# Kernel optimization log

Hardware: AMD Instinct MI355X
Metric: run time of the kernel (lower is better)

Reference implementation:

```python
import jax, jax.numpy as jnp
import numpy as np

B, S, D, N, H, K = 32, 512, 2048, 16, 128, 64
EPS = 1e-6


def setup_inputs() -> dict:
    key = jax.random.key(0)
    ks = jax.random.split(key, 8)
    # glorot-uniform-like scale for the (D, N, H) attention kernels
    kern_scale = (6.0 / (D + H)) ** 0.5
    down_sd = 1.0 / K  # matches module: mean 0, sd = 1/downsampling_k
    q = jax.random.normal(ks[0], (B, S, D), dtype=jnp.float32)
    k = jax.random.normal(ks[1], (B, S, D), dtype=jnp.float32)
    v = jax.random.normal(ks[2], (B, S, D), dtype=jnp.float32)
    query_kernel = jax.random.uniform(ks[3], (D, N, H), jnp.float32, -kern_scale, kern_scale)
    key_kernel = jax.random.uniform(ks[4], (D, N, H), jnp.float32, -kern_scale, kern_scale)
    value_kernel = jax.random.uniform(ks[5], (D, N, H), jnp.float32, -kern_scale, kern_scale)
    key_down = down_sd * jax.random.normal(ks[6], (K, S), dtype=jnp.float32)
    value_down = down_sd * jax.random.normal(ks[7], (K, S), dtype=jnp.float32)
    return dict(q=q, k=k, v=v, query_kernel=query_kernel, key_kernel=key_kernel,
                value_kernel=value_kernel, key_down=key_down, value_down=value_down)


def reference(q, k, v, query_kernel, key_kernel, value_kernel, key_down, value_down):
    # Linformer-style downsampling of keys/values along the sequence axis: [B,S,D] -> [B,K,D]
    key_ds = jnp.einsum('ks,bsd->bkd', key_down, k)
    val_ds = jnp.einsum('ks,bsd->bkd', value_down, v)
    # Per-head projections
    queries = jnp.einsum('bqd,dnh->bqnh', q, query_kernel)   # [B,S,N,H]
    keys = jnp.einsum('bkd,dnh->bknh', key_ds, key_kernel)   # [B,K,N,H]
    values = jnp.einsum('bkd,dnh->bknh', val_ds, value_kernel)  # [B,K,N,H]
    # Kernelized linear attention with elu+1 feature map (mask=False branch)
    phi_q = jax.nn.elu(queries) + 1.0
    phi_k = jax.nn.elu(keys) + 1.0
    s = jnp.einsum('bknd,bknh->bndh', phi_k, values)  # [B,N,H,H]
    z = jnp.sum(phi_k, axis=1)                        # [B,N,H]
    qs = jnp.einsum('bqnd,bndh->bqnh', phi_q, s)      # [B,S,N,H]
    qz = jnp.einsum('bqnd,bnd->bqn', phi_q, z) + EPS  # [B,S,N]
    a_v = qs / qz[..., None]
    return a_v.reshape(B, S, N * H)
```

## Files before the change

kernel.cpp:

```cpp
#include <hip/hip_runtime.h>
#include <cstdint>
#include <cstddef>

typedef float f32x4 __attribute__((ext_vector_type(4)));
typedef short s16x8 __attribute__((ext_vector_type(8)));
typedef unsigned short u16;

#define EPS 1e-6f

__device__ __forceinline__ u16 f2bf(float f) {
    unsigned u = __float_as_uint(f);
    u += 0x7FFFu + ((u >> 16) & 1u);
    return (u16)(u >> 16);
}
__device__ __forceinline__ float bf2f(u16 u) {
    return __uint_as_float(((unsigned)u) << 16);
}

typedef const __attribute__((address_space(1))) void cg_void;
typedef __attribute__((address_space(3))) void l_void;
__device__ __forceinline__ void async16(void* dst_lds, const void* src_g) {
    __builtin_amdgcn_global_load_lds((cg_void*)src_g, (l_void*)dst_lds, 16, 0, 0);
}

#define BARRIER() do { asm volatile("" ::: "memory"); \
                       __builtin_amdgcn_s_barrier();  \
                       asm volatile("" ::: "memory"); } while (0)

__global__ __launch_bounds__(256) void prep_down(
    const float* __restrict__ q, u16* __restrict__ qb,
    const float* __restrict__ w0, const float* __restrict__ w1,
    const float* __restrict__ w2, u16* __restrict__ o0,
    u16* __restrict__ o1, u16* __restrict__ o2,
    const float* __restrict__ kin, const float* __restrict__ vin,
    const float* __restrict__ wdk, const float* __restrict__ wdv,
    u16* __restrict__ kds, u16* __restrict__ vds)
{
    __shared__ __align__(16) u16 At[64 * 32];
    __shared__ __align__(16) u16 Bt[128 * 40];
    __shared__ u16 tl[32][33];
    const int bid = blockIdx.x;
    const int tid = threadIdx.x;

    if (bid < 1024) {
        const int sel = bid >> 9, rem = bid & 511;
        const int b = rem >> 4, d0 = (rem & 15) << 7;
        const float* x  = sel ? vin : kin;
        const float* wd = sel ? wdv : wdk;
        u16* outp       = sel ? vds : kds;
        int w = tid >> 6, l = tid & 63, l16 = l & 15, k8 = l >> 4;
        f32x4 acc[4][2] = {};
        for (int s0 = 0; s0 < 512; s0 += 32) {
            __syncthreads();
            for (int c = tid; c < 512; c += 256) {
                int kkr = c >> 3, sc = (c & 7) << 2;
                float4 f = *(const float4*)&wd[kkr * 512 + s0 + sc];
                u16* dst = &At[kkr * 32 + sc];
                dst[0] = f2bf(f.x); dst[1] = f2bf(f.y); dst[2] = f2bf(f.z); dst[3] = f2bf(f.w);
            }
            for (int c = tid; c < 512; c += 256) {
                int sp = c >> 5, dq = (c & 31) << 2;
                int srow = sp << 1;
                const float* xp = &x[((size_t)(b * 512) + s0 + srow) * 2048 + d0 + dq];
                float4 f0 = *(const float4*)xp;
                float4 f1 = *(const float4*)(xp + 2048);
                unsigned p0 = (unsigned)f2bf(f0.x) | ((unsigned)f2bf(f1.x) << 16);
                unsigned p1 = (unsigned)f2bf(f0.y) | ((unsigned)f2bf(f1.y) << 16);
                unsigned p2 = (unsigned)f2bf(f0.z) | ((unsigned)f2bf(f1.z) << 16);
                unsigned p3 = (unsigned)f2bf(f0.w) | ((unsigned)f2bf(f1.w) << 16);
                *(unsigned*)&Bt[(dq + 0) * 40 + srow] = p0;
                *(unsigned*)&Bt[(dq + 1) * 40 + srow] = p1;
                *(unsigned*)&Bt[(dq + 2) * 40 + srow] = p2;
                *(unsigned*)&Bt[(dq + 3) * 40 + srow] = p3;
            }
            __syncthreads();
            s16x8 af[4], bfr[2];
            #pragma unroll
            for (int fm = 0; fm < 4; ++fm)
                af[fm] = *(const s16x8*)&At[(fm * 16 + l16) * 32 + k8 * 8];
            #pragma unroll
            for (int fn = 0; fn < 2; ++fn)
                bfr[fn] = *(const s16x8*)&Bt[(w * 32 + fn * 16 + l16) * 40 + k8 * 8];
            #pragma unroll
            for (int fm = 0; fm < 4; ++fm)
                #pragma unroll
                for (int fn = 0; fn < 2; ++fn)
                    acc[fm][fn] = __builtin_amdgcn_mfma_f32_16x16x32_bf16(af[fm], bfr[fn], acc[fm][fn], 0, 0, 0);
        }
        #pragma unroll
        for (int fm = 0; fm < 4; ++fm)
            #pragma unroll
            for (int fn = 0; fn < 2; ++fn)
                #pragma unroll
                for (int j = 0; j < 4; ++j) {
                    int r = fm * 16 + k8 * 4 + j;
                    int c = w * 32 + fn * 16 + l16;
                    outp[((size_t)(b * 64 + r)) * 2048 + d0 + c] = f2bf(acc[fm][fn][j]);
                }
    } else if (bid < 13312) {
        int wb = bid - 1024;
        int which = wb >> 12;
        int t = wb & 4095;
        const float* in = which == 0 ? w0 : which == 1 ? w1 : w2;
        u16* out        = which == 0 ? o0 : which == 1 ? o1 : o2;
        int bx = (t & 63) * 32, by = (t >> 6) * 32;
        int tx = tid & 31, ty = tid >> 5;
        for (int i = ty; i < 32; i += 8)
            tl[i][tx] = f2bf(in[(size_t)(by + i) * 2048 + bx + tx]);
        __syncthreads();
        for (int i = ty; i < 32; i += 8)
            out[(size_t)(bx + i) * 2048 + by + tx] = tl[tx][i];
    } else {
        int cb = bid - 13312;
        size_t base = (size_t)cb * 256 + tid;
        #pragma unroll
        for (int it = 0; it < 8; ++it) {
            size_t i = base + (size_t)it * 1048576;
            float4 f = ((const float4*)q)[i];
            ushort4 o;
            o.x = f2bf(f.x); o.y = f2bf(f.y); o.z = f2bf(f.z); o.w = f2bf(f.w);
            ((ushort4*)qb)[i] = o;
        }
    }
}

__global__ __launch_bounds__(512, 2) void gemm256_elu(
    const u16* __restrict__ A, const u16* __restrict__ BT,
    u16* __restrict__ C, int M, int N, int K)
{
    __shared__ __align__(16) u16 lds[8][8192];
    const int tid = threadIdx.x;
    const int w = tid >> 6, l = tid & 63;
    const int wm = w >> 2, wn = w & 3;
    const int l16 = l & 15, k8 = l >> 4;
    const int NT = K >> 6;

    const int nbn = N >> 8;
    const int nwg = gridDim.x;
    int wg = blockIdx.x;
    if ((nwg & 7) == 0) wg = (wg & 7) * (nwg >> 3) + (wg >> 3);
    const int row0 = (wg / nbn) << 8, col0 = (wg % nbn) << 8;

    const int lr  = l >> 3;
    const int scb = (((l & 7) ^ lr) << 4);
    const int swzr = (l16 & 7) << 4;

#define PANEL(s, m, h) (&lds[((s) << 2) | ((m) << 1) | (h)][0])

#define STG(pan, G, prow0, kk0) do {                                             \
        _Pragma("unroll")                                                        \
        for (int i_ = 0; i_ < 2; ++i_) {                                         \
            int seg_ = w + (i_ << 3);                                            \
            const u16* src_ = (G) + (size_t)((prow0) + (seg_ << 3) + lr) * K     \
                              + (kk0) + (scb >> 1);                              \
            async16((pan) + (seg_ << 9), src_);                                  \
        } } while (0)

#define LDA(slot, mh) do { const u16* p_ = PANEL(slot, 0, mh);                   \
        _Pragma("unroll")                                                        \
        for (int fm_ = 0; fm_ < 4; ++fm_)                                        \
        _Pragma("unroll")                                                        \
        for (int ks_ = 0; ks_ < 2; ++ks_)                                        \
            Af[fm_][ks_] = *(const s16x8*)(p_ + (wm * 64 + fm_ * 16 + l16) * 64  \
                           + (((ks_ * 64 + k8 * 16) ^ swzr) >> 1)); } while (0)

#define LDB(slot, nh, dst) do { const u16* p_ = PANEL(slot, 1, nh);              \
        _Pragma("unroll")                                                        \
        for (int fn_ = 0; fn_ < 2; ++fn_)                                        \
        _Pragma("unroll")                                                        \
        for (int ks_ = 0; ks_ < 2; ++ks_)                                        \
            dst[fn_][ks_] = *(const s16x8*)(p_ + (wn * 32 + fn_ * 16 + l16) * 64 \
                           + (((ks_ * 64 + k8 * 16) ^ swzr) >> 1)); } while (0)

#define MM(mh, nh, BF) do {                                                      \
        __builtin_amdgcn_s_setprio(1);                                           \
        _Pragma("unroll")                                                        \
        for (int fm_ = 0; fm_ < 4; ++fm_)                                        \
        _Pragma("unroll")                                                        \
        for (int fn_ = 0; fn_ < 2; ++fn_)                                        \
        _Pragma("unroll")                                                        \
        for (int ks_ = 0; ks_ < 2; ++ks_)                                        \
            acc[mh][nh][fm_][fn_] = __builtin_amdgcn_mfma_f32_16x16x32_bf16(     \
                Af[fm_][ks_], BF[fn_][ks_], acc[mh][nh][fm_][fn_], 0, 0, 0);     \
        __builtin_amdgcn_s_setprio(0); } while (0)

#define TILE(t, cur, nxt, BFc, BFn) do {                                         \
                                                                        \
        LDA(cur, 0);                                                             \
        if ((t) + 1 < NT) STG(PANEL(nxt, 0, 1), A, row0 + 128, ((t) + 1) << 6);  \
        BARRIER(); MM(0, 0, BFc); BARRIER();                                     \
                                                                        \
        LDB(cur, 1, Bf1);                                                        \
        if ((t) + 2 < NT) STG(PANEL(cur, 0, 0), A, row0, ((t) + 2) << 6);        \
        BARRIER(); MM(0, 1, Bf1); BARRIER();                                     \
                                                                        \
        LDA(cur, 1);                                                             \
        if ((t) + 2 < NT) STG(PANEL(cur, 1, 0), BT, col0, ((t) + 2) << 6);       \
        BARRIER(); MM(1, 1, Bf1); BARRIER();                                     \
                                                                        \
        if ((t) + 2 < NT) STG(PANEL(cur, 1, 1), BT, col0 + 128, ((t) + 2) << 6); \
        BARRIER(); MM(1, 0, BFc);                                                \
        if ((t) == NT - 2)     asm volatile("s_waitcnt vmcnt(0)" ::: "memory");  \
        else if ((t) < NT - 2) asm volatile("s_waitcnt vmcnt(6)" ::: "memory");  \
        BARRIER();                                                               \
        if ((t) + 1 < NT) LDB(nxt, 0, BFn);       \
    } while (0)

    f32x4 acc[2][2][4][2] = {};
    s16x8 Af[4][2], Bf0a[2][2], Bf0b[2][2], Bf1[2][2];

    STG(PANEL(0, 0, 0), A,  row0,       0);
    STG(PANEL(0, 1, 0), BT, col0,       0);
    STG(PANEL(0, 1, 1), BT, col0 + 128, 0);
    STG(PANEL(0, 0, 1), A,  row0 + 128, 0);
    STG(PANEL(1, 0, 0), A,  row0,       64);
    STG(PANEL(1, 1, 0), BT, col0,       64);
    STG(PANEL(1, 1, 1), BT, col0 + 128, 64);
    asm volatile("s_waitcnt vmcnt(6)" ::: "memory");
    BARRIER();
    LDB(0, 0, Bf0a);

    for (int t = 0; t < NT; t += 2) {
        TILE(t,     0, 1, Bf0a, Bf0b);
        TILE(t + 1, 1, 0, Bf0b, Bf0a);
    }
#undef PANEL
#undef STG
#undef LDA
#undef LDB
#undef MM
#undef TILE

    #pragma unroll
    for (int mh = 0; mh < 2; ++mh)
        #pragma unroll
        for (int fm = 0; fm < 4; ++fm)
            #pragma unroll
            for (int j = 0; j < 4; ++j) {
                int r = row0 + mh * 128 + wm * 64 + fm * 16 + k8 * 4 + j;
                size_t rb = (size_t)r * N;
                #pragma unroll
                for (int nh = 0; nh < 2; ++nh)
                    #pragma unroll
                    for (int fn = 0; fn < 2; ++fn) {
                        int c = col0 + nh * 128 + wn * 32 + fn * 16 + l16;
                        float x = acc[mh][nh][fm][fn][j];
                        x = x > 0.0f ? x + 1.0f : __expf(x);
                        C[rb + c] = f2bf(x);
                    }
            }
}

__global__ __launch_bounds__(256) void gemm128_dual(
    const u16* __restrict__ A0, const u16* __restrict__ B0, u16* __restrict__ C0,
    const u16* __restrict__ A1, const u16* __restrict__ B1, u16* __restrict__ C1)
{
    const u16* A  = blockIdx.z ? A1 : A0;
    const u16* BT = blockIdx.z ? B1 : B0;
    u16* C        = blockIdx.z ? C1 : C0;
    const bool elu = (blockIdx.z == 0);
    const int K = 2048;

    __shared__ __align__(16) u16 lds[2][8192];
    const int tid = threadIdx.x;
    const int w = tid >> 6, l = tid & 63;
    const int wm = w >> 1, wn = w & 1;
    const int l16 = l & 15, k8 = l >> 4;
    const int sr = (w << 4) + (l >> 2);
    const int sc = (l & 3) << 3;
    const int row0 = blockIdx.y * 128, col0 = blockIdx.x * 128;
    const int nk = K >> 5;
    f32x4 acc[4][4] = {};

#define STAGE(buf, kt) do {                                                        \
        int kk0 = (kt) << 5;                                                       \
        _Pragma("unroll")                                                          \
        for (int i = 0; i < 2; ++i) {                                              \
            const u16* ga = A + (size_t)(row0 + i * 64 + sr) * K + kk0 + sc;       \
            async16(&lds[buf][i * 2048 + (w << 9)], ga);                           \
            const u16* gb = BT + (size_t)(col0 + i * 64 + sr) * K + kk0 + sc;      \
            async16(&lds[buf][4096 + i * 2048 + (w << 9)], gb);                    \
        }                                                                          \
    } while (0)

    STAGE(0, 0);
    asm volatile("s_waitcnt vmcnt(0)" ::: "memory");
    __syncthreads();
    int cur = 0;
    for (int kt = 0; kt < nk; ++kt) {
        if (kt + 1 < nk) STAGE(cur ^ 1, kt + 1);
        s16x8 af[4], bfr[4];
        const u16* Ab = &lds[cur][0];
        const u16* Bb = &lds[cur][4096];
        #pragma unroll
        for (int fm = 0; fm < 4; ++fm)
            af[fm] = *(const s16x8*)&Ab[((wm << 6) + (fm << 4) + l16) * 32 + (k8 << 3)];
        #pragma unroll
        for (int fn = 0; fn < 4; ++fn)
            bfr[fn] = *(const s16x8*)&Bb[((wn << 6) + (fn << 4) + l16) * 32 + (k8 << 3)];
        #pragma unroll
        for (int fm = 0; fm < 4; ++fm)
            #pragma unroll
            for (int fn = 0; fn < 4; ++fn)
                acc[fm][fn] = __builtin_amdgcn_mfma_f32_16x16x32_bf16(af[fm], bfr[fn], acc[fm][fn], 0, 0, 0);
        __syncthreads();
        cur ^= 1;
    }
#undef STAGE

    #pragma unroll
    for (int fm = 0; fm < 4; ++fm)
        #pragma unroll
        for (int j = 0; j < 4; ++j) {
            int r = row0 + (wm << 6) + (fm << 4) + (k8 << 2) + j;
            size_t rbase = (size_t)r * 2048;
            #pragma unroll
            for (int fn = 0; fn < 4; ++fn) {
                int c = col0 + (wn << 6) + (fn << 4) + l16;
                float x = acc[fm][fn][j];
                if (elu) x = x > 0.0f ? x + 1.0f : __expf(x);
                C[rbase + c] = f2bf(x);
            }
        }
}

__global__ __launch_bounds__(256) void sz_kernel(
    const u16* __restrict__ phik, const u16* __restrict__ vals,
    u16* __restrict__ sT, float* __restrict__ z)
{
    int b = blockIdx.x >> 4, n = blockIdx.x & 15;
    __shared__ __align__(16) u16 pk[64 * 128];
    __shared__ __align__(16) u16 vv[64 * 128];
    int tid = threadIdx.x;
    for (int i = tid; i < 1024; i += 256) {
        int r = i >> 4, c8 = (i & 15) << 3;
        size_t g = ((size_t)(b * 64 + r)) * 2048 + n * 128 + c8;
        ((s16x8*)pk)[i] = *(const s16x8*)&phik[g];
        ((s16x8*)vv)[i] = *(const s16x8*)&vals[g];
    }
    __syncthreads();
    if (tid < 128) {
        float s = 0.0f;
        for (int kk = 0; kk < 64; ++kk) s += bf2f(pk[kk * 128 + tid]);
        z[((size_t)(b * 16 + n)) * 128 + tid] = s;
    }
    int hg = tid >> 4, dg = tid & 15;
    int h0 = hg * 8, d0 = dg * 8;
    float acc[8][8] = {};
    for (int kk = 0; kk < 64; ++kk) {
        s16x8 vr = *(const s16x8*)&vv[kk * 128 + h0];
        s16x8 pr = *(const s16x8*)&pk[kk * 128 + d0];
        float va[8], pa[8];
        #pragma unroll
        for (int i = 0; i < 8; ++i) { va[i] = bf2f((u16)vr[i]); pa[i] = bf2f((u16)pr[i]); }
        #pragma unroll
        for (int i = 0; i < 8; ++i)
            #pragma unroll
            for (int j = 0; j < 8; ++j)
                acc[i][j] += va[i] * pa[j];
    }
    size_t base = ((size_t)(b * 16 + n)) * 16384;
    #pragma unroll
    for (int i = 0; i < 8; ++i) {
        u16 row[8];
        #pragma unroll
        for (int j = 0; j < 8; ++j) row[j] = f2bf(acc[i][j]);
        *(s16x8*)&sT[base + (size_t)(h0 + i) * 128 + d0] = *(s16x8*)row;
    }
}

__global__ __launch_bounds__(256) void qs_kernel(
    const u16* __restrict__ phiq, const u16* __restrict__ sT,
    const float* __restrict__ z, float* __restrict__ out)
{
    const int gb = blockIdx.x;
    const int rb = gb & 3, bn = gb >> 2;
    const int b = bn >> 4, n = bn & 15;
    __shared__ __align__(16) u16 Blds[128 * 128];
    const int tid = threadIdx.x;
    const int w = tid >> 6, l = tid & 63;
    const int l16 = l & 15, k8 = l >> 4;

    {
        const u16* base = sT + (size_t)bn * 16384;
        #pragma unroll
        for (int r0 = 0; r0 < 128; r0 += 16) {
            int row = r0 + (w << 2) + (l >> 4);
            int scb = (((l & 15) ^ (row & 7)) << 4);
            async16(&Blds[(r0 + (w << 2)) * 128], base + (size_t)row * 128 + (scb >> 1));
        }
    }

    const size_t arow0 = (size_t)(b * 512 + rb * 128);
    s16x8 Af[2][4];
    #pragma unroll
    for (int fm = 0; fm < 2; ++fm)
        #pragma unroll
        for (int ks = 0; ks < 4; ++ks) {
            int row = (w << 5) + (fm << 4) + l16;
            Af[fm][ks] = *(const s16x8*)(phiq + (arow0 + row) * 2048 + n * 128
                                         + (ks << 5) + (k8 << 3));
        }

    s16x8 Bz[4];
    #pragma unroll
    for (int ks = 0; ks < 4; ++ks) {
        const float* zp = z + (size_t)bn * 128 + (ks << 5) + (k8 << 3);
        float4 f0 = *(const float4*)zp;
        float4 f1 = *(const float4*)(zp + 4);
        u16 tmp[8] = { f2bf(f0.x), f2bf(f0.y), f2bf(f0.z), f2bf(f0.w),
                       f2bf(f1.x), f2bf(f1.y), f2bf(f1.z), f2bf(f1.w) };
        Bz[ks] = *(const s16x8*)tmp;
    }

    f32x4 accz[2] = {};
    #pragma unroll
    for (int fm = 0; fm < 2; ++fm)
        #pragma unroll
        for (int ks = 0; ks < 4; ++ks)
            accz[fm] = __builtin_amdgcn_mfma_f32_16x16x32_bf16(Af[fm][ks], Bz[ks], accz[fm], 0, 0, 0);

    asm volatile("s_waitcnt vmcnt(0)" ::: "memory");
    BARRIER();

    const int swz = (l16 & 7) << 4;
    f32x4 acc[2][8] = {};
    #pragma unroll
    for (int fn = 0; fn < 8; ++fn) {
        s16x8 Bf[4];
        #pragma unroll
        for (int ks = 0; ks < 4; ++ks)
            Bf[ks] = *(const s16x8*)&Blds[((fn << 4) + l16) * 128
                                          + ((((ks << 6) + (k8 << 4)) ^ swz) >> 1)];
        #pragma unroll
        for (int fm = 0; fm < 2; ++fm)
            #pragma unroll
            for (int ks = 0; ks < 4; ++ks)
                acc[fm][fn] = __builtin_amdgcn_mfma_f32_16x16x32_bf16(Af[fm][ks], Bf[ks], acc[fm][fn], 0, 0, 0);
    }

    #pragma unroll
    for (int fm = 0; fm < 2; ++fm)
        #pragma unroll
        for (int j = 0; j < 4; ++j) {
            int row = (w << 5) + (fm << 4) + (k8 << 2) + j;
            float rq = 1.0f / (accz[fm][j] + EPS);
            size_t ob = (arow0 + row) * 2048 + n * 128;
            #pragma unroll
            for (int fn = 0; fn < 8; ++fn)
                out[ob + (fn << 4) + l16] = acc[fm][fn][j] * rq;
        }
}

extern "C" void kernel_launch(void* const* d_in, const int* in_sizes, int n_in,
                              void* d_out, int out_size, void* d_ws, size_t ws_size,
                              hipStream_t stream) {
    (void)in_sizes; (void)n_in; (void)out_size; (void)ws_size;
    const float* q   = (const float*)d_in[0];
    const float* k   = (const float*)d_in[1];
    const float* v   = (const float*)d_in[2];
    const float* wq  = (const float*)d_in[3];
    const float* wk  = (const float*)d_in[4];
    const float* wv  = (const float*)d_in[5];
    const float* kdw = (const float*)d_in[6];
    const float* vdw = (const float*)d_in[7];
    float* out = (float*)d_out;

    char* p = (char*)d_ws;
    u16* qb   = (u16*)p; p += (size_t)16384 * 2048 * 2;
    u16* wqT  = (u16*)p; p += (size_t)2048 * 2048 * 2;
    u16* wkT  = (u16*)p; p += (size_t)2048 * 2048 * 2;
    u16* wvT  = (u16*)p; p += (size_t)2048 * 2048 * 2;
    u16* kds  = (u16*)p; p += (size_t)2048 * 2048 * 2;
    u16* vds  = (u16*)p; p += (size_t)2048 * 2048 * 2;
    u16* phiq = (u16*)p; p += (size_t)16384 * 2048 * 2;
    u16* phik = (u16*)p; p += (size_t)2048 * 2048 * 2;
    u16* vals = (u16*)p; p += (size_t)2048 * 2048 * 2;
    u16* sT   = (u16*)p; p += (size_t)512 * 128 * 128 * 2;
    float* z  = (float*)p; p += (size_t)512 * 128 * 4;

    prep_down<<<17408, 256, 0, stream>>>(q, qb, wq, wk, wv, wqT, wkT, wvT,
                                         k, v, kdw, vdw, kds, vds);
    gemm128_dual<<<dim3(16, 16, 2), 256, 0, stream>>>(kds, wkT, phik, vds, wvT, vals);
    gemm256_elu<<<512, 512, 0, stream>>>(qb, wqT, phiq, 16384, 2048, 2048);
    sz_kernel<<<512, 256, 0, stream>>>(phik, vals, sT, z);
    qs_kernel<<<2048, 256, 0, stream>>>(phiq, sT, z, out);
}
```

Baseline: 372.3 us.

## Double-buffer downsampling GEMM with register prefetch, swizzle LDS, vectorize transpose stores

The downsampling branch of prep_down now prefetches the next K-slice of weights and activations into registers while MFMAs run on the current LDS buffer, then writes the next slice into a second LDS buffer. This removes one barrier per iteration and hides global load latency. An XOR swizzle on the Bt column index is meant to reduce LDS bank conflicts. The weight transpose path now writes 4 bf16 values per thread as short4 stores instead of scalar stores. The cost is doubled LDS for At/Bt and more registers held live for the prefetch.

```diff
diff --git a/kernel.cpp b/kernel.cpp
--- a/kernel.cpp
+++ b/kernel.cpp
@@ -36,8 +36,8 @@
     const float* __restrict__ wdk, const float* __restrict__ wdv,
     u16* __restrict__ kds, u16* __restrict__ vds)
 {
-    __shared__ __align__(16) u16 At[64 * 32];
-    __shared__ __align__(16) u16 Bt[128 * 40];
+    __shared__ __align__(16) u16 At[2][64 * 32];
+    __shared__ __align__(16) u16 Bt[2][128 * 40];
     __shared__ u16 tl[32][33];
     const int bid = blockIdx.x;
     const int tid = threadIdx.x;
@@ -48,45 +48,65 @@
         const float* x  = sel ? vin : kin;
         const float* wd = sel ? wdv : wdk;
         u16* outp       = sel ? vds : kds;
-        int w = tid >> 6, l = tid & 63, l16 = l & 15, k8 = l >> 4;
+        const int w = tid >> 6, l = tid & 63, l16 = l & 15, k8 = l >> 4;
         f32x4 acc[4][2] = {};
-        for (int s0 = 0; s0 < 512; s0 += 32) {
-            __syncthreads();
-            for (int c = tid; c < 512; c += 256) {
-                int kkr = c >> 3, sc = (c & 7) << 2;
-                float4 f = *(const float4*)&wd[kkr * 512 + s0 + sc];
-                u16* dst = &At[kkr * 32 + sc];
-                dst[0] = f2bf(f.x); dst[1] = f2bf(f.y); dst[2] = f2bf(f.z); dst[3] = f2bf(f.w);
-            }
-            for (int c = tid; c < 512; c += 256) {
-                int sp = c >> 5, dq = (c & 31) << 2;
-                int srow = sp << 1;
-                const float* xp = &x[((size_t)(b * 512) + s0 + srow) * 2048 + d0 + dq];
-                float4 f0 = *(const float4*)xp;
-                float4 f1 = *(const float4*)(xp + 2048);
-                unsigned p0 = (unsigned)f2bf(f0.x) | ((unsigned)f2bf(f1.x) << 16);
-                unsigned p1 = (unsigned)f2bf(f0.y) | ((unsigned)f2bf(f1.y) << 16);
-                unsigned p2 = (unsigned)f2bf(f0.z) | ((unsigned)f2bf(f1.z) << 16);
-                unsigned p3 = (unsigned)f2bf(f0.w) | ((unsigned)f2bf(f1.w) << 16);
-                *(unsigned*)&Bt[(dq + 0) * 40 + srow] = p0;
-                *(unsigned*)&Bt[(dq + 1) * 40 + srow] = p1;
-                *(unsigned*)&Bt[(dq + 2) * 40 + srow] = p2;
-                *(unsigned*)&Bt[(dq + 3) * 40 + srow] = p3;
-            }
-            __syncthreads();
+        float4 wf[2], xf0[2], xf1[2];
+
+#define DLOAD(s0) do {                                                            \
+        _Pragma("unroll")                                                         \
+        for (int u = 0; u < 2; ++u) {                                             \
+            int c = tid + (u << 8);                                               \
+            wf[u] = *(const float4*)&wd[(c >> 3) * 512 + (s0) + ((c & 7) << 2)];  \
+            const float* xp = &x[((size_t)(b * 512) + (s0) + ((c >> 5) << 1))     \
+                                 * 2048 + d0 + ((c & 31) << 2)];                  \
+            xf0[u] = *(const float4*)xp;                                          \
+            xf1[u] = *(const float4*)(xp + 2048);                                 \
+        } } while (0)
+
+#define DWRITE(bufv) do {                                                         \
+        _Pragma("unroll")                                                         \
+        for (int u = 0; u < 2; ++u) {                                             \
+            int c = tid + (u << 8);                                               \
+            int kkr = c >> 3, sc = (c & 7) << 2;                                  \
+            u16* dst = &At[bufv][kkr * 32 + sc];                                  \
+            dst[0] = f2bf(wf[u].x); dst[1] = f2bf(wf[u].y);                       \
+            dst[2] = f2bf(wf[u].z); dst[3] = f2bf(wf[u].w);                       \
+            int dq = (c & 31) << 2;                                               \
+            int col = (((c >> 5) << 1)) ^ ((c & 3) << 3);                         \
+            unsigned p0 = (unsigned)f2bf(xf0[u].x) | ((unsigned)f2bf(xf1[u].x) << 16); \
+            unsigned p1 = (unsigned)f2bf(xf0[u].y) | ((unsigned)f2bf(xf1[u].y) << 16); \
+            unsigned p2 = (unsigned)f2bf(xf0[u].z) | ((unsigned)f2bf(xf1[u].z) << 16); \
+            unsigned p3 = (unsigned)f2bf(xf0[u].w) | ((unsigned)f2bf(xf1[u].w) << 16); \
+            *(unsigned*)&Bt[bufv][(dq + 0) * 40 + col] = p0;                      \
+            *(unsigned*)&Bt[bufv][(dq + 1) * 40 + col] = p1;                      \
+            *(unsigned*)&Bt[bufv][(dq + 2) * 40 + col] = p2;                      \
+            *(unsigned*)&Bt[bufv][(dq + 3) * 40 + col] = p3;                      \
+        } } while (0)
+
+        DLOAD(0);
+        DWRITE(0);
+        __syncthreads();
+        for (int t = 0; t < 16; ++t) {
+            const int cb = t & 1;
+            if (t < 15) DLOAD((t + 1) << 5);
             s16x8 af[4], bfr[2];
             #pragma unroll
             for (int fm = 0; fm < 4; ++fm)
-                af[fm] = *(const s16x8*)&At[(fm * 16 + l16) * 32 + k8 * 8];
+                af[fm] = *(const s16x8*)&At[cb][(fm * 16 + l16) * 32 + k8 * 8];
             #pragma unroll
             for (int fn = 0; fn < 2; ++fn)
-                bfr[fn] = *(const s16x8*)&Bt[(w * 32 + fn * 16 + l16) * 40 + k8 * 8];
+                bfr[fn] = *(const s16x8*)&Bt[cb][(w * 32 + fn * 16 + l16) * 40
+                                                 + ((k8 ^ (l16 >> 2)) << 3)];
             #pragma unroll
             for (int fm = 0; fm < 4; ++fm)
                 #pragma unroll
                 for (int fn = 0; fn < 2; ++fn)
                     acc[fm][fn] = __builtin_amdgcn_mfma_f32_16x16x32_bf16(af[fm], bfr[fn], acc[fm][fn], 0, 0, 0);
+            if (t < 15) DWRITE(cb ^ 1);
+            __syncthreads();
         }
+#undef DLOAD
+#undef DWRITE
         #pragma unroll
         for (int fm = 0; fm < 4; ++fm)
             #pragma unroll
@@ -108,8 +128,12 @@
         for (int i = ty; i < 32; i += 8)
             tl[i][tx] = f2bf(in[(size_t)(by + i) * 2048 + bx + tx]);
         __syncthreads();
-        for (int i = ty; i < 32; i += 8)
-            out[(size_t)(bx + i) * 2048 + by + tx] = tl[tx][i];
+        int row = tid >> 3, qd = tid & 7;
+        u16 o[4];
+        #pragma unroll
+        for (int m = 0; m < 4; ++m) o[m] = tl[4 * qd + m][row];
+        *(short4*)&out[(size_t)(bx + row) * 2048 + by + 4 * qd] =
+            make_short4((short)o[0], (short)o[1], (short)o[2], (short)o[3]);
     } else {
         int cb = bid - 13312;
         size_t base = (size_t)cb * 256 + tid;
@@ -185,25 +209,21 @@
         __builtin_amdgcn_s_setprio(0); } while (0)
 
 #define TILE(t, cur, nxt, BFc, BFn) do {                                         \
-                                                                        \
         LDA(cur, 0);                                                             \
         if ((t) + 1 < NT) STG(PANEL(nxt, 0, 1), A, row0 + 128, ((t) + 1) << 6);  \
         BARRIER(); MM(0, 0, BFc); BARRIER();                                     \
-                                                                        \
         LDB(cur, 1, Bf1);                                                        \
         if ((t) + 2 < NT) STG(PANEL(cur, 0, 0), A, row0, ((t) + 2) << 6);        \
         BARRIER(); MM(0, 1, Bf1); BARRIER();                                     \
-                                                                        \
         LDA(cur, 1);                                                             \
         if ((t) + 2 < NT) STG(PANEL(cur, 1, 0), BT, col0, ((t) + 2) << 6);       \
         BARRIER(); MM(1, 1, Bf1); BARRIER();                                     \
-                                                                        \
         if ((t) + 2 < NT) STG(PANEL(cur, 1, 1), BT, col0 + 128, ((t) + 2) << 6); \
         BARRIER(); MM(1, 0, BFc);                                                \
         if ((t) == NT - 2)     asm volatile("s_waitcnt vmcnt(0)" ::: "memory");  \
         else if ((t) < NT - 2) asm volatile("s_waitcnt vmcnt(6)" ::: "memory");  \
         BARRIER();                                                               \
-        if ((t) + 1 < NT) LDB(nxt, 0, BFn);       \
+        if ((t) + 1 < NT) LDB(nxt, 0, BFn);                                      \
     } while (0)
 
     f32x4 acc[2][2][4][2] = {};
```

Result: slower. 391.2 us (+5.1%).
